# Kernel optimization log

Measured on AMD Instinct MI355X. Metric: run time of the kernel, lower is better.

## Reference

```python
import jax, jax.numpy as jnp
import numpy as np

D_MODEL = 1024
NUM_HEAD = 16
D_HEAD = D_MODEL // NUM_HEAD


def setup_inputs() -> dict:
    key = jax.random.key(0)
    kx, kq, kk, kv, ko = jax.random.split(key, 5)
    x = jax.random.normal(kx, (2, 2048, D_MODEL), dtype=jnp.float32)
    p_q = jax.random.normal(kq, (D_MODEL, D_MODEL), dtype=jnp.float32)
    p_k = jax.random.normal(kk, (D_MODEL, D_MODEL), dtype=jnp.float32)
    p_v = jax.random.normal(kv, (D_MODEL, D_MODEL), dtype=jnp.float32)
    p_o = jax.random.normal(ko, (D_MODEL, D_MODEL), dtype=jnp.float32)
    return {"x": x, "p_q": p_q, "p_k": p_k, "p_v": p_v, "p_o": p_o}


def reference(x, p_q, p_k, p_v, p_o):
    B, S, _ = x.shape
    # project: weight viewed as [H, d_head, d_model]; out[b,h,s,d] = sum_m x[b,s,m] W[h,d,m]
    wq = p_q.reshape(NUM_HEAD, D_HEAD, D_MODEL)
    wk = p_k.reshape(NUM_HEAD, D_HEAD, D_MODEL)
    wv = p_v.reshape(NUM_HEAD, D_HEAD, D_MODEL)
    q = jnp.einsum('bsm,hdm->bhsd', x, wq)
    k = jnp.einsum('bsm,hdm->bhsd', x, wk)
    v = jnp.einsum('bsm,hdm->bhsd', x, wv)
    # full causal attention, scores scaled by 1/sqrt(d_head)
    scores = jnp.einsum('bhqd,bhkd->bhqk', q, k) / jnp.sqrt(jnp.float32(D_HEAD))
    causal = jnp.tril(jnp.ones((S, S), dtype=bool))
    scores = jnp.where(causal, scores, -jnp.inf)
    attn = jax.nn.softmax(scores, axis=-1)
    out = jnp.einsum('bhqk,bhkd->bhqd', attn, v)
    out = out.transpose(0, 2, 1, 3).reshape(B, S, D_MODEL)  # [B,S,H*d_head]
    # output proj: einsum '... d1, d2 d1 -> ... d2' == out @ p_o.T
    return jnp.einsum('bsm,nm->bsn', out, p_o)
```

## Files before the change

kernel.cpp:

```cpp
#include <hip/hip_runtime.h>
#include <stdint.h>

#define D_MODEL 1024
#define SEQ     2048
#define NHEAD   16
#define BATCH   2
#define NROWS   (BATCH*SEQ)

typedef _Float16 f16;
typedef _Float16 f16x8 __attribute__((ext_vector_type(8)));
typedef _Float16 f16x4 __attribute__((ext_vector_type(4)));
typedef __fp16   h16x2 __attribute__((ext_vector_type(2)));
typedef float    f32x4 __attribute__((ext_vector_type(4)));

#define MFMA16 __builtin_amdgcn_mfma_f32_16x16x32_f16

__device__ __forceinline__ void gload16(const void* g, void* l) {
  __builtin_amdgcn_global_load_lds(
      (const __attribute__((address_space(1))) void*)g,
      (__attribute__((address_space(3))) void*)l, 16, 0, 0);
}

__device__ __forceinline__ int pkh2(float a, float b) {
  union { h16x2 h; int i; } u;
  u.h = __builtin_amdgcn_cvt_pkrtz(a, b);
  return u.i;
}

__global__ void split4_kernel(const float* __restrict__ in, f16* __restrict__ hi,
                              f16* __restrict__ lo, int n4, float scale) {
  int i = blockIdx.x * blockDim.x + threadIdx.x;
  if (i >= n4) return;
  float4 v = reinterpret_cast<const float4*>(in)[i];
  v.x *= scale; v.y *= scale; v.z *= scale; v.w *= scale;
  f16x4 h, l4;
  h[0] = (f16)v.x; h[1] = (f16)v.y; h[2] = (f16)v.z; h[3] = (f16)v.w;
  l4[0] = (f16)(v.x - (float)h[0]);
  l4[1] = (f16)(v.y - (float)h[1]);
  l4[2] = (f16)(v.z - (float)h[2]);
  l4[3] = (f16)(v.w - (float)h[3]);
  *reinterpret_cast<f16x4*>(hi + 4*(size_t)i) = h;
  *reinterpret_cast<f16x4*>(lo + 4*(size_t)i) = l4;
}

__global__ void prep_w_kernel(const float* __restrict__ pq, const float* __restrict__ pk,
                              const float* __restrict__ pv, const float* __restrict__ po,
                              f16* __restrict__ wq_hi, f16* __restrict__ wq_lo,
                              f16* __restrict__ wk_hi, f16* __restrict__ wk_lo,
                              f16* __restrict__ wv_h,  f16* __restrict__ wo_h,
                              int n4, float qscale) {
  int i = blockIdx.x * blockDim.x + threadIdx.x;
  if (i >= n4) return;
  {
    float4 v = reinterpret_cast<const float4*>(pq)[i];
    v.x *= qscale; v.y *= qscale; v.z *= qscale; v.w *= qscale;
    f16x4 h, l4;
    h[0] = (f16)v.x; h[1] = (f16)v.y; h[2] = (f16)v.z; h[3] = (f16)v.w;
    l4[0] = (f16)(v.x - (float)h[0]); l4[1] = (f16)(v.y - (float)h[1]);
    l4[2] = (f16)(v.z - (float)h[2]); l4[3] = (f16)(v.w - (float)h[3]);
    *reinterpret_cast<f16x4*>(wq_hi + 4*(size_t)i) = h;
    *reinterpret_cast<f16x4*>(wq_lo + 4*(size_t)i) = l4;
  }
  {
    float4 v = reinterpret_cast<const float4*>(pk)[i];
    f16x4 h, l4;
    h[0] = (f16)v.x; h[1] = (f16)v.y; h[2] = (f16)v.z; h[3] = (f16)v.w;
    l4[0] = (f16)(v.x - (float)h[0]); l4[1] = (f16)(v.y - (float)h[1]);
    l4[2] = (f16)(v.z - (float)h[2]); l4[3] = (f16)(v.w - (float)h[3]);
    *reinterpret_cast<f16x4*>(wk_hi + 4*(size_t)i) = h;
    *reinterpret_cast<f16x4*>(wk_lo + 4*(size_t)i) = l4;
  }
  {
    float4 v = reinterpret_cast<const float4*>(pv)[i];
    f16x4 h;
    h[0] = (f16)v.x; h[1] = (f16)v.y; h[2] = (f16)v.z; h[3] = (f16)v.w;
    *reinterpret_cast<f16x4*>(wv_h + 4*(size_t)i) = h;
  }
  {
    float4 v = reinterpret_cast<const float4*>(po)[i];
    f16x4 h;
    h[0] = (f16)v.x; h[1] = (f16)v.y; h[2] = (f16)v.z; h[3] = (f16)v.w;
    *reinterpret_cast<f16x4*>(wo_h + 4*(size_t)i) = h;
  }
}

template<bool F32_OUT, bool COLCHUNK>
__global__ __launch_bounds__(256, 2)
void gemm_nt(const f16* __restrict__ Ahi,
             const f16* __restrict__ Bhi,
             f16* __restrict__ Chi, float* __restrict__ Cf,
             int M, int N, int K)
{
  constexpr int B_OFF  = 8192;
  constexpr int STRIDE = 12288;
  __shared__ __align__(16) char smem[2 * STRIDE];

  const int tid = threadIdx.x;
  const int w = tid >> 6, l = tid & 63;
  const int wr = (w >> 1) * 64;
  const int wc = (w & 1) * 32;

  const int gx = gridDim.x, gy = gridDim.y;
  const int nwg = gx * gy;
  const int flat = blockIdx.y * gx + blockIdx.x;
  const int swz = (flat & 7) * (nwg >> 3) + (flat >> 3);
  const int bxn = COLCHUNK ? (swz / gy) : (swz % gx);
  const int byn = COLCHUNK ? (swz % gy) : (swz / gx);
  const int bm = byn * 128, bn = bxn * 64;

  f32x4 acc[4][2] = {};

  const int srow = tid >> 2;
  const int schunk = 8 * (((tid & 3) ^ ((srow >> 1) & 3)));

  auto stage = [&](int kt) {
    char* dst = smem + (kt & 1) * STRIDE;
    const int k0 = kt * 32;
    const f16* ga = Ahi + (size_t)(bm + srow) * K + k0 + schunk;
    gload16(ga,        dst + (w << 10));
    gload16(ga + 64*K, dst + 4096 + (w << 10));
    const f16* gb = Bhi + (size_t)(bn + srow) * K + k0 + schunk;
    gload16(gb,        dst + B_OFF + (w << 10));
  };

  const int nkt = K >> 5;
  stage(0);

  for (int kt = 0; kt < nkt; kt++) {
    if (kt + 1 < nkt) {
      stage(kt + 1);
      asm volatile("s_waitcnt vmcnt(3)" ::: "memory");
    } else {
      asm volatile("s_waitcnt vmcnt(0)" ::: "memory");
    }
    __builtin_amdgcn_s_barrier();

    const char* buf = smem + (kt & 1) * STRIDE;
    const int ar = (l & 15);
    const int ak = 16 * ((l >> 4) ^ ((ar >> 1) & 3));
    f16x8 a_hi[4];
#pragma unroll
    for (int mi = 0; mi < 4; mi++)
      a_hi[mi] = *(const f16x8*)(buf + (size_t)(wr + mi*16 + ar) * 64 + ak);
    __builtin_amdgcn_s_setprio(1);
#pragma unroll
    for (int ni = 0; ni < 2; ni++) {
      f16x8 b_hi = *(const f16x8*)(buf + B_OFF + (size_t)(wc + ni*16 + ar) * 64 + ak);
#pragma unroll
      for (int mi = 0; mi < 4; mi++)
        acc[mi][ni] = MFMA16(a_hi[mi], b_hi, acc[mi][ni], 0, 0, 0);
    }
    __builtin_amdgcn_s_setprio(0);
    __builtin_amdgcn_s_barrier();
  }

  const int crow0 = bm + wr + (l >> 4) * 4;
  const int ccol0 = bn + wc + (l & 15);
#pragma unroll
  for (int mi = 0; mi < 4; mi++) {
#pragma unroll
    for (int ni = 0; ni < 2; ni++) {
#pragma unroll
      for (int j = 0; j < 4; j++) {
        size_t idx = (size_t)(crow0 + mi*16 + j) * N + (ccol0 + ni*16);
        float v = acc[mi][ni][j];
        if (F32_OUT) Cf[idx] = v;
        else         Chi[idx] = (f16)v;
      }
    }
  }
}

__global__ __launch_bounds__(256, 2)
void gemm_qk(const f16* __restrict__ Ahi, const f16* __restrict__ Alo,
             const f16* __restrict__ Bqh, const f16* __restrict__ Bql,
             const f16* __restrict__ Bkh, const f16* __restrict__ Bkl,
             f16* __restrict__ Qh, f16* __restrict__ Qlo2,
             f16* __restrict__ Kh, f16* __restrict__ Klo2)
{
  constexpr int N = D_MODEL, K = D_MODEL;
  constexpr int STRIDE = 32768;
  __shared__ __align__(16) char smem[2 * STRIDE];

  const int tid = threadIdx.x;
  const int w = tid >> 6, l = tid & 63;
  const int wr = (w >> 1) * 64;
  const int wc = (w & 1) * 32;

  const int flat = blockIdx.y * 16 + blockIdx.x;
  const int swz = (flat & 7) * 64 + (flat >> 3);
  const int bm = (swz / 16) * 128, bn = (swz % 16) * 64;

  f32x4 accQ[4][2] = {}, accK[4][2] = {};

  const int srow = tid >> 2;
  const int schunk = 8 * (((tid & 3) ^ ((srow >> 1) & 3)));

  auto stage = [&](int kt) {
    char* dst = smem + (kt & 1) * STRIDE;
    const int k0 = kt * 32;
    const f16* ga = Ahi + (size_t)(bm + srow) * K + k0 + schunk;
    gload16(ga,        dst + (w << 10));
    gload16(ga + 64*K, dst + 4096 + (w << 10));
    const f16* gal = Alo + (size_t)(bm + srow) * K + k0 + schunk;
    gload16(gal,        dst + 8192 + (w << 10));
    gload16(gal + 64*K, dst + 12288 + (w << 10));
    const size_t bo = (size_t)(bn + srow) * K + k0 + schunk;
    gload16(Bqh + bo, dst + 16384 + (w << 10));
    gload16(Bql + bo, dst + 20480 + (w << 10));
    gload16(Bkh + bo, dst + 24576 + (w << 10));
    gload16(Bkl + bo, dst + 28672 + (w << 10));
  };

  const int nkt = K >> 5;
  stage(0);

  for (int kt = 0; kt < nkt; kt++) {
    if (kt + 1 < nkt) {
      stage(kt + 1);
      asm volatile("s_waitcnt vmcnt(8)" ::: "memory");
    } else {
      asm volatile("s_waitcnt vmcnt(0)" ::: "memory");
    }
    __builtin_amdgcn_s_barrier();

    const char* buf = smem + (kt & 1) * STRIDE;
    const int ar = (l & 15);
    const int ak = 16 * ((l >> 4) ^ ((ar >> 1) & 3));
    f16x8 a_hi[4], a_lo[4];
#pragma unroll
    for (int mi = 0; mi < 4; mi++) {
      a_hi[mi] = *(const f16x8*)(buf + (size_t)(wr + mi*16 + ar) * 64 + ak);
      a_lo[mi] = *(const f16x8*)(buf + 8192 + (size_t)(wr + mi*16 + ar) * 64 + ak);
    }
    __builtin_amdgcn_s_setprio(1);
#pragma unroll
    for (int ni = 0; ni < 2; ni++) {
      const int bo = (wc + ni*16 + ar) * 64 + ak;
      f16x8 bqh = *(const f16x8*)(buf + 16384 + bo);
      f16x8 bql = *(const f16x8*)(buf + 20480 + bo);
      f16x8 bkh = *(const f16x8*)(buf + 24576 + bo);
      f16x8 bkl = *(const f16x8*)(buf + 28672 + bo);
#pragma unroll
      for (int mi = 0; mi < 4; mi++) {
        accQ[mi][ni] = MFMA16(a_hi[mi], bqh, accQ[mi][ni], 0, 0, 0);
        accQ[mi][ni] = MFMA16(a_hi[mi], bql, accQ[mi][ni], 0, 0, 0);
        accQ[mi][ni] = MFMA16(a_lo[mi], bqh, accQ[mi][ni], 0, 0, 0);
        accK[mi][ni] = MFMA16(a_hi[mi], bkh, accK[mi][ni], 0, 0, 0);
        accK[mi][ni] = MFMA16(a_hi[mi], bkl, accK[mi][ni], 0, 0, 0);
        accK[mi][ni] = MFMA16(a_lo[mi], bkh, accK[mi][ni], 0, 0, 0);
      }
    }
    __builtin_amdgcn_s_setprio(0);
    __builtin_amdgcn_s_barrier();
  }

  const int crow0 = bm + wr + (l >> 4) * 4;
  const int ccol0 = bn + wc + (l & 15);
#pragma unroll
  for (int mi = 0; mi < 4; mi++) {
#pragma unroll
    for (int ni = 0; ni < 2; ni++) {
#pragma unroll
      for (int j = 0; j < 4; j++) {
        size_t idx = (size_t)(crow0 + mi*16 + j) * N + (ccol0 + ni*16);
        float qv = accQ[mi][ni][j];
        f16 qh = (f16)qv;
        Qh[idx] = qh;  Qlo2[idx] = (f16)(qv - (float)qh);
        float kv = accK[mi][ni][j];
        f16 kh = (f16)kv;
        Kh[idx] = kh;  Klo2[idx] = (f16)(kv - (float)kh);
      }
    }
  }
}

__global__ __launch_bounds__(512, 4)
void attn_kernel(const f16* __restrict__ Qhi, const f16* __restrict__ Qlo,
                 const f16* __restrict__ Khi, const f16* __restrict__ Klo,
                 const f16* __restrict__ VT, f16* __restrict__ Out)
{
  __shared__ __align__(16) char smem[49152];

  const int tid = threadIdx.x, w = tid >> 6, l = tid & 63;
  const int g = l >> 4, q4 = l & 15;
  const int wi = w & 3, grp = w >> 2;
  const int flat = blockIdx.x;
  const int xcd = flat & 7, slot = flat >> 3;
  const int bh = xcd * 4 + (slot >> 4);
  const int c = slot & 15;
  const int b = bh >> 4, h = bh & 15;
  const int bS = b * SEQ;
  const size_t hoff = (size_t)h * 64;
  const int T  = 64 - 2 * c;
  const int P1 = 2 * c + 2;
  const int P2 = 31 - 2 * c;

  int qw = (grp ? (31 - c) : c) * 64 + wi * 16;

  f16x8 qh[2], ql[2];
  auto loadQ = [&]() {
#pragma unroll
    for (int ks = 0; ks < 2; ks++) {
      const size_t base = (size_t)(bS + qw + q4) * D_MODEL + hoff + ks * 32 + g * 8;
      qh[ks] = *(const f16x8*)(Qhi + base);
      ql[ks] = *(const f16x8*)(Qlo + base);
    }
  };
  loadQ();

  f32x4 o[4] = {};
  float m_run = -INFINITY, l_run = 0.f;

  const int k_src = 8 * ((l & 7) ^ (l >> 3));
  const int v_src = 8 * ((l & 3) ^ ((l >> 2) & 3));
  const int rowloc = w * 8 + (l >> 3);

  const int idx_lo = (q4 + 32 * (g & 1)) * 4;
  const int idx_hi = idx_lo + 64;
  const bool upper = (l >= 32);

  auto stage64 = [&](int t) {
    const int kv0 = t * 64;
    char* dst = smem + (t & 1) * 24576;
    const size_t krow = (size_t)(bS + kv0 + rowloc) * D_MODEL + hoff + k_src;
    gload16(Khi + krow, dst + (w << 10));
    gload16(Klo + krow, dst + 8192 + (w << 10));
    const size_t vrow = (hoff + rowloc) * (size_t)NROWS + bS + kv0 + k_src;
    gload16(VT + vrow, dst + 16384 + (w << 10));
  };

  auto compute64 = [&](int t) {
    const char* buf = smem + (t & 1) * 24576;
    const int kv0 = t * 64;

    f32x4 s[4] = {};
    __builtin_amdgcn_s_setprio(1);
#pragma unroll
    for (int ni = 0; ni < 4; ni++) {
      const int row = ni * 16 + q4;
#pragma unroll
      for (int ks = 0; ks < 2; ks++) {
        const int boff = row * 128 + 16 * ((ks * 4 + g) ^ (row & 7));
        f16x8 kh8 = *(const f16x8*)(buf + boff);
        f16x8 kl8 = *(const f16x8*)(buf + 8192 + boff);
        s[ni] = MFMA16(kh8, qh[ks], s[ni], 0, 0, 0);
        s[ni] = MFMA16(kh8, ql[ks], s[ni], 0, 0, 0);
        s[ni] = MFMA16(kl8, qh[ks], s[ni], 0, 0, 0);
      }
    }
    __builtin_amdgcn_s_setprio(0);

    const bool need_mask = (kv0 + 63) > qw;
    const int q_abs = qw + q4;
    float p[4][4];
    float pm = -INFINITY;
#pragma unroll
    for (int ni = 0; ni < 4; ni++)
#pragma unroll
      for (int j = 0; j < 4; j++) {
        float v = s[ni][j];
        if (need_mask && (kv0 + ni * 16 + 4 * g + j) > q_abs) v = -INFINITY;
        p[ni][j] = v;
        pm = fmaxf(pm, v);
      }
    pm = fmaxf(pm, __shfl_xor(pm, 16));
    pm = fmaxf(pm, __shfl_xor(pm, 32));

    if (!__all(pm - m_run <= 8.0f)) {
      const float mn = fmaxf(m_run, pm);
      const float sc2 = __builtin_amdgcn_exp2f(m_run - mn);
      m_run = mn;
      l_run *= sc2;
#pragma unroll
      for (int nd = 0; nd < 4; nd++)
#pragma unroll
        for (int j = 0; j < 4; j++) o[nd][j] *= sc2;
    }
    float ps = 0.f;
#pragma unroll
    for (int ni = 0; ni < 4; ni++)
#pragma unroll
      for (int j = 0; j < 4; j++) {
        const float e = __builtin_amdgcn_exp2f(p[ni][j] - m_run);
        p[ni][j] = e;
        ps += e;
      }
    ps += __shfl_xor(ps, 16);
    ps += __shfl_xor(ps, 32);
    l_run += ps;

    f16x8 pa[2];
#pragma unroll
    for (int h2 = 0; h2 < 2; h2++) {
      const int pk0 = pkh2(p[2*h2][0],   p[2*h2][1]);
      const int pk1 = pkh2(p[2*h2][2],   p[2*h2][3]);
      const int pk2 = pkh2(p[2*h2+1][0], p[2*h2+1][1]);
      const int pk3 = pkh2(p[2*h2+1][2], p[2*h2+1][3]);
      const int b0l = __builtin_amdgcn_ds_bpermute(idx_lo, pk0);
      const int b2l = __builtin_amdgcn_ds_bpermute(idx_lo, pk2);
      const int b1l = __builtin_amdgcn_ds_bpermute(idx_lo, pk1);
      const int b3l = __builtin_amdgcn_ds_bpermute(idx_lo, pk3);
      const int b0h = __builtin_amdgcn_ds_bpermute(idx_hi, pk0);
      const int b2h = __builtin_amdgcn_ds_bpermute(idx_hi, pk2);
      const int b1h = __builtin_amdgcn_ds_bpermute(idx_hi, pk1);
      const int b3h = __builtin_amdgcn_ds_bpermute(idx_hi, pk3);
      union { int u[4]; f16x8 v; } pu;
      pu.u[0] = upper ? b2l : b0l;
      pu.u[1] = upper ? b3l : b1l;
      pu.u[2] = upper ? b2h : b0h;
      pu.u[3] = upper ? b3h : b1h;
      pa[h2] = pu.v;
    }

    __builtin_amdgcn_s_setprio(1);
#pragma unroll
    for (int nd = 0; nd < 4; nd++) {
      const int d = nd * 16 + q4;
#pragma unroll
      for (int h2 = 0; h2 < 2; h2++) {
        f16x8 bv = *(const f16x8*)(buf + 16384 + d * 128 + 16 * ((h2 * 4 + g) ^ (d & 7)));
        o[nd] = MFMA16(bv, pa[h2], o[nd], 0, 0, 0);
      }
    }
    __builtin_amdgcn_s_setprio(0);
  };

  auto stage32 = [&](int t) {
    const int kv0 = t * 32;
    char* sb = smem + (t & 3) * 12288;
    if (w < 4) {
      const f16* src = (w < 2) ? Khi : Klo;
      char* dstc = sb + ((w < 2) ? 0 : 4096);
      const int wi2 = w & 1;
#pragma unroll
      for (int gi = 0; gi < 2; gi++) {
        const int sub = 2 * wi2 + gi;
        const int row = 8 * sub + (l >> 3);
        gload16(src + (size_t)(bS + kv0 + row) * D_MODEL + hoff + k_src,
                dstc + sub * 1024);
      }
    } else if (w < 6) {
      const int wi2 = w - 4;
#pragma unroll
      for (int gi = 0; gi < 2; gi++) {
        const int sub = 2 * wi2 + gi;
        const int drow = 16 * sub + (l >> 2);
        gload16(VT + (hoff + drow) * (size_t)NROWS + bS + kv0 + v_src,
                sb + 8192 + sub * 1024);
      }
    }
  };

  auto compute32 = [&](int t) {
    const char* sb = smem + (t & 3) * 12288;
    const int kv0 = t * 32;

    f32x4 s[2] = {};
    __builtin_amdgcn_s_setprio(1);
#pragma unroll
    for (int ni = 0; ni < 2; ni++) {
      const int row = ni * 16 + q4;
#pragma unroll
      for (int ks = 0; ks < 2; ks++) {
        const int boff = row * 128 + 16 * ((ks * 4 + g) ^ (row & 7));
        f16x8 kh8 = *(const f16x8*)(sb + boff);
        f16x8 kl8 = *(const f16x8*)(sb + 4096 + boff);
        s[ni] = MFMA16(kh8, qh[ks], s[ni], 0, 0, 0);
        s[ni] = MFMA16(kh8, ql[ks], s[ni], 0, 0, 0);
        s[ni] = MFMA16(kl8, qh[ks], s[ni], 0, 0, 0);
      }
    }
    __builtin_amdgcn_s_setprio(0);

    const bool need_mask = (kv0 + 31) > qw;
    const int q_abs = qw + q4;
    float p[2][4];
    float pm = -INFINITY;
#pragma unroll
    for (int ni = 0; ni < 2; ni++)
#pragma unroll
      for (int j = 0; j < 4; j++) {
        float v = s[ni][j];
        if (need_mask && (kv0 + ni * 16 + 4 * g + j) > q_abs) v = -INFINITY;
        p[ni][j] = v;
        pm = fmaxf(pm, v);
      }
    pm = fmaxf(pm, __shfl_xor(pm, 16));
    pm = fmaxf(pm, __shfl_xor(pm, 32));

    if (!__all(pm - m_run <= 8.0f)) {
      const float mn = fmaxf(m_run, pm);
      const float sc2 = __builtin_amdgcn_exp2f(m_run - mn);
      m_run = mn;
      l_run *= sc2;
#pragma unroll
      for (int nd = 0; nd < 4; nd++)
#pragma unroll
        for (int j = 0; j < 4; j++) o[nd][j] *= sc2;
    }
    float ps = 0.f;
#pragma unroll
    for (int ni = 0; ni < 2; ni++)
#pragma unroll
      for (int j = 0; j < 4; j++) {
        const float e = __builtin_amdgcn_exp2f(p[ni][j] - m_run);
        p[ni][j] = e;
        ps += e;
      }
    ps += __shfl_xor(ps, 16);
    ps += __shfl_xor(ps, 32);
    l_run += ps;

    const int pk0 = pkh2(p[0][0], p[0][1]);
    const int pk1 = pkh2(p[0][2], p[0][3]);
    const int pk2 = pkh2(p[1][0], p[1][1]);
    const int pk3 = pkh2(p[1][2], p[1][3]);
    const int b0l = __builtin_amdgcn_ds_bpermute(idx_lo, pk0);
    const int b2l = __builtin_amdgcn_ds_bpermute(idx_lo, pk2);
    const int b1l = __builtin_amdgcn_ds_bpermute(idx_lo, pk1);
    const int b3l = __builtin_amdgcn_ds_bpermute(idx_lo, pk3);
    const int b0h = __builtin_amdgcn_ds_bpermute(idx_hi, pk0);
    const int b2h = __builtin_amdgcn_ds_bpermute(idx_hi, pk2);
    const int b1h = __builtin_amdgcn_ds_bpermute(idx_hi, pk1);
    const int b3h = __builtin_amdgcn_ds_bpermute(idx_hi, pk3);
    union { int u[4]; f16x8 v; } pu;
    pu.u[0] = upper ? b2l : b0l;
    pu.u[1] = upper ? b3l : b1l;
    pu.u[2] = upper ? b2h : b0h;
    pu.u[3] = upper ? b3h : b1h;
    const f16x8 pa = pu.v;

    __builtin_amdgcn_s_setprio(1);
#pragma unroll
    for (int nd = 0; nd < 4; nd++) {
      const int d = nd * 16 + q4;
      f16x8 bv = *(const f16x8*)(sb + 8192 + d * 64 + 16 * (g ^ (d & 3)));
      o[nd] = MFMA16(bv, pa, o[nd], 0, 0, 0);
    }
    __builtin_amdgcn_s_setprio(0);
  };

  stage64(0);
  for (int t = 0; t <= c; t++) {
    if (t + 1 <= c) {
      stage64(t + 1);
      asm volatile("s_waitcnt vmcnt(3)" ::: "memory");
    } else {
      asm volatile("s_waitcnt vmcnt(0)" ::: "memory");
    }
    __builtin_amdgcn_s_barrier();
    compute64(t);
    __builtin_amdgcn_s_barrier();
  }

  if (grp == 0) {
    const float inv = 1.0f / l_run;
    const size_t rowb = (size_t)(bS + qw + q4) * D_MODEL + hoff;
#pragma unroll
    for (int nd = 0; nd < 4; nd++) {
      f16x4 v;
#pragma unroll
      for (int j = 0; j < 4; j++) v[j] = (f16)(o[nd][j] * inv);
      *reinterpret_cast<f16x4*>(Out + rowb + nd * 16 + 4 * g) = v;
    }
    qw = (31 - c) * 64 + wi * 16;
    loadQ();
#pragma unroll
    for (int nd = 0; nd < 4; nd++)
#pragma unroll
      for (int j = 0; j < 4; j++) o[nd][j] = 0.f;
    m_run = -INFINITY;
    l_run = 0.f;
  }

  stage32(P1);
  stage32(P1 + 1);
  for (int j = 0; j < P2; j++) {
    const int u = P1 + 2 * j;
    const bool st = (u + 3) < T;
    if (st) { stage32(u + 2); stage32(u + 3); }
    if (st) asm volatile("s_waitcnt vmcnt(4)" ::: "memory");
    else    asm volatile("s_waitcnt vmcnt(0)" ::: "memory");
    __builtin_amdgcn_s_barrier();
    compute32(u + grp);
    __builtin_amdgcn_s_barrier();
  }

  if (grp == 0) {
    float* mb = (float*)smem + wi * 1152 + l * 18;
#pragma unroll
    for (int nd = 0; nd < 4; nd++)
#pragma unroll
      for (int j = 0; j < 4; j++) mb[nd * 4 + j] = o[nd][j];
    mb[16] = m_run;
    mb[17] = l_run;
  }
  __syncthreads();
  if (grp == 1) {
    const float* mb = (const float*)smem + wi * 1152 + l * 18;
    const float m2 = mb[16], l2 = mb[17];
    const float mm = fmaxf(m_run, m2);
    const float a1 = __builtin_amdgcn_exp2f(m_run - mm);
    const float a2 = __builtin_amdgcn_exp2f(m2 - mm);
    const float inv = 1.0f / (l_run * a1 + l2 * a2);
    const size_t rowb = (size_t)(bS + qw + q4) * D_MODEL + hoff;
#pragma unroll
    for (int nd = 0; nd < 4; nd++) {
      f16x4 v;
#pragma unroll
      for (int j = 0; j < 4; j++)
        v[j] = (f16)((o[nd][j] * a1 + mb[nd * 4 + j] * a2) * inv);
      *reinterpret_cast<f16x4*>(Out + rowb + nd * 16 + 4 * g) = v;
    }
  }
}

extern "C" void kernel_launch(void* const* d_in, const int* in_sizes, int n_in,
                              void* d_out, int out_size, void* d_ws, size_t ws_size,
                              hipStream_t stream) {
  const float* x  = (const float*)d_in[0];
  const float* pq = (const float*)d_in[1];
  const float* pk = (const float*)d_in[2];
  const float* pv = (const float*)d_in[3];
  const float* po = (const float*)d_in[4];
  float* out = (float*)d_out;

  char* ws = (char*)d_ws;
  size_t off = 0;
  auto alloc = [&](size_t elems) {
    f16* p = (f16*)(ws + off);
    off += ((elems * 2 + 255) & ~(size_t)255);
    return p;
  };
  f16* x_hi  = alloc((size_t)NROWS * D_MODEL);
  f16* x_lo  = alloc((size_t)NROWS * D_MODEL);
  f16* wq_hi = alloc((size_t)D_MODEL * D_MODEL);
  f16* wq_lo = alloc((size_t)D_MODEL * D_MODEL);
  f16* wk_hi = alloc((size_t)D_MODEL * D_MODEL);
  f16* wk_lo = alloc((size_t)D_MODEL * D_MODEL);
  f16* wv_h  = alloc((size_t)D_MODEL * D_MODEL);
  f16* wo_h  = alloc((size_t)D_MODEL * D_MODEL);
  f16* q_hi  = alloc((size_t)NROWS * D_MODEL);
  f16* q_lo  = alloc((size_t)NROWS * D_MODEL);
  f16* k_hi  = alloc((size_t)NROWS * D_MODEL);
  f16* k_lo  = alloc((size_t)NROWS * D_MODEL);
  f16* vt    = alloc((size_t)NROWS * D_MODEL);
  f16* ao    = alloc((size_t)NROWS * D_MODEL);

  const int n4x = NROWS * D_MODEL / 4;
  const int n4w = D_MODEL * D_MODEL / 4;
  const float qscale = 0.125f * 1.44269504088896f;
  split4_kernel<<<n4x/256, 256, 0, stream>>>(x, x_hi, x_lo, n4x, 1.0f);
  prep_w_kernel<<<n4w/256, 256, 0, stream>>>(pq, pk, pv, po,
                                             wq_hi, wq_lo, wk_hi, wk_lo, wv_h, wo_h,
                                             n4w, qscale);

  gemm_qk<<<dim3(16, 32), 256, 0, stream>>>(x_hi, x_lo, wq_hi, wq_lo, wk_hi, wk_lo,
                                            q_hi, q_lo, k_hi, k_lo);
  dim3 gv(NROWS/64, D_MODEL/128);
  gemm_nt<false, true><<<gv, 256, 0, stream>>>(wv_h, x_hi, vt, nullptr, D_MODEL, NROWS, D_MODEL);

  attn_kernel<<<dim3(512), 512, 0, stream>>>(q_hi, q_lo, k_hi, k_lo, vt, ao);

  dim3 gg(D_MODEL/64, NROWS/128);
  gemm_nt<true, false><<<gg, 256, 0, stream>>>(ao, wo_h, nullptr, out, NROWS, D_MODEL, D_MODEL);
}
```

Measured before the change: 166.1 us.

## Fuse V projection into QK GEMM kernel with transposed LDS epilogue

Adds the V projection to the combined Q/K GEMM so the A tiles (x hi/lo) are loaded once and reused for all three projections, and drops the separate V GEMM launch. V is accumulated from the hi part only, then written transposed through shared memory to the VT layout the attention kernel expects. LDS per block grows, and so do register pressure from the third accumulator set and the wait count, which may hurt occupancy at two blocks per CU.

```diff
diff --git a/kernel.cpp b/kernel.cpp
--- a/kernel.cpp
+++ b/kernel.cpp
@@ -172,14 +172,16 @@
 }
 
 __global__ __launch_bounds__(256, 2)
-void gemm_qk(const f16* __restrict__ Ahi, const f16* __restrict__ Alo,
-             const f16* __restrict__ Bqh, const f16* __restrict__ Bql,
-             const f16* __restrict__ Bkh, const f16* __restrict__ Bkl,
-             f16* __restrict__ Qh, f16* __restrict__ Qlo2,
-             f16* __restrict__ Kh, f16* __restrict__ Klo2)
+void gemm_qkv(const f16* __restrict__ Ahi, const f16* __restrict__ Alo,
+              const f16* __restrict__ Bqh, const f16* __restrict__ Bql,
+              const f16* __restrict__ Bkh, const f16* __restrict__ Bkl,
+              const f16* __restrict__ Bvh,
+              f16* __restrict__ Qh, f16* __restrict__ Qlo2,
+              f16* __restrict__ Kh, f16* __restrict__ Klo2,
+              f16* __restrict__ VT)
 {
   constexpr int N = D_MODEL, K = D_MODEL;
-  constexpr int STRIDE = 32768;
+  constexpr int STRIDE = 36864;
   __shared__ __align__(16) char smem[2 * STRIDE];
 
   const int tid = threadIdx.x;
@@ -191,7 +193,7 @@
   const int swz = (flat & 7) * 64 + (flat >> 3);
   const int bm = (swz / 16) * 128, bn = (swz % 16) * 64;
 
-  f32x4 accQ[4][2] = {}, accK[4][2] = {};
+  f32x4 accQ[4][2] = {}, accK[4][2] = {}, accV[4][2] = {};
 
   const int srow = tid >> 2;
   const int schunk = 8 * (((tid & 3) ^ ((srow >> 1) & 3)));
@@ -210,6 +212,7 @@
     gload16(Bql + bo, dst + 20480 + (w << 10));
     gload16(Bkh + bo, dst + 24576 + (w << 10));
     gload16(Bkl + bo, dst + 28672 + (w << 10));
+    gload16(Bvh + bo, dst + 32768 + (w << 10));
   };
 
   const int nkt = K >> 5;
@@ -218,7 +221,7 @@
   for (int kt = 0; kt < nkt; kt++) {
     if (kt + 1 < nkt) {
       stage(kt + 1);
-      asm volatile("s_waitcnt vmcnt(8)" ::: "memory");
+      asm volatile("s_waitcnt vmcnt(9)" ::: "memory");
     } else {
       asm volatile("s_waitcnt vmcnt(0)" ::: "memory");
     }
@@ -241,6 +244,7 @@
       f16x8 bql = *(const f16x8*)(buf + 20480 + bo);
       f16x8 bkh = *(const f16x8*)(buf + 24576 + bo);
       f16x8 bkl = *(const f16x8*)(buf + 28672 + bo);
+      f16x8 bvh = *(const f16x8*)(buf + 32768 + bo);
 #pragma unroll
       for (int mi = 0; mi < 4; mi++) {
         accQ[mi][ni] = MFMA16(a_hi[mi], bqh, accQ[mi][ni], 0, 0, 0);
@@ -249,6 +253,7 @@
         accK[mi][ni] = MFMA16(a_hi[mi], bkh, accK[mi][ni], 0, 0, 0);
         accK[mi][ni] = MFMA16(a_hi[mi], bkl, accK[mi][ni], 0, 0, 0);
         accK[mi][ni] = MFMA16(a_lo[mi], bkh, accK[mi][ni], 0, 0, 0);
+        accV[mi][ni] = MFMA16(a_hi[mi], bvh, accV[mi][ni], 0, 0, 0);
       }
     }
     __builtin_amdgcn_s_setprio(0);
@@ -271,6 +276,30 @@
         f16 kh = (f16)kv;
         Kh[idx] = kh;  Klo2[idx] = (f16)(kv - (float)kh);
       }
+    }
+  }
+
+  {
+    f16* tl = (f16*)smem;
+#pragma unroll
+    for (int mi = 0; mi < 4; mi++) {
+#pragma unroll
+      for (int ni = 0; ni < 2; ni++) {
+        f16x4 v;
+#pragma unroll
+        for (int j = 0; j < 4; j++) v[j] = (f16)accV[mi][ni][j];
+        const int m_l = wc + ni*16 + (l & 15);
+        const int n_l = wr + mi*16 + ((l >> 4) << 2);
+        *reinterpret_cast<f16x4*>(tl + m_l*136 + n_l) = v;
+      }
+    }
+    __syncthreads();
+    const int m_l = tid >> 2, cg = tid & 3;
+    const size_t vbase = (size_t)(bn + m_l) * NROWS + bm + cg*32;
+#pragma unroll
+    for (int k2 = 0; k2 < 4; k2++) {
+      f16x8 v = *reinterpret_cast<const f16x8*>(tl + m_l*136 + cg*32 + k2*8);
+      *reinterpret_cast<f16x8*>(VT + vbase + k2*8) = v;
     }
   }
 }
@@ -656,10 +685,8 @@
                                              wq_hi, wq_lo, wk_hi, wk_lo, wv_h, wo_h,
                                              n4w, qscale);
 
-  gemm_qk<<<dim3(16, 32), 256, 0, stream>>>(x_hi, x_lo, wq_hi, wq_lo, wk_hi, wk_lo,
-                                            q_hi, q_lo, k_hi, k_lo);
-  dim3 gv(NROWS/64, D_MODEL/128);
-  gemm_nt<false, true><<<gv, 256, 0, stream>>>(wv_h, x_hi, vt, nullptr, D_MODEL, NROWS, D_MODEL);
+  gemm_qkv<<<dim3(16, 32), 256, 0, stream>>>(x_hi, x_lo, wq_hi, wq_lo, wk_hi, wk_lo,
+                                             wv_h, q_hi, q_lo, k_hi, k_lo, vt);
 
   attn_kernel<<<dim3(512), 512, 0, stream>>>(q_hi, q_lo, k_hi, k_lo, vt, ao);
 
```

New measurement: 157.0 us. -5.4%, faster.
